# Optimization experiments

Hardware: AMD Instinct MI355X
Metric: run time of the kernel (lower is better)

## Reference

```python
import jax, jax.numpy as jnp
import numpy as np

# QuadraticConv2DTranspose reconstruction:
#   1) bed-of-nails upsample by stride s (pixels at i*s, zeros elsewhere), padded by k-1
#      so a VALID conv yields output H*s x W*s ('same' transpose-conv geometry)
#   2) per-(pixel, in_channel) flattened k*k patch p (K=k*k values)
#   3) quadratic features: upper-triangular outer products p_i*p_j (K*(K+1)/2 terms),
#      plus linear terms p (K) and a bias term 1  -> L = 55 for k=3
#   4) contract features against flat_kernel [1,1,L,Cin,Cout]

KH = 3            # kernel height/width
STRIDE = 2
KK = KH * KH      # flattened patch size per channel = 9
L = KK * (KK + 1) // 2 + KK + 1  # 45 quad + 9 linear + 1 bias = 55
B, H, W, CIN, COUT = 8, 32, 32, 64, 64


def setup_inputs() -> dict:
    key = jax.random.key(0)
    k1, k2 = jax.random.split(key)
    x = jax.random.normal(k1, (B, H, W, CIN), dtype=jnp.float32)
    flat_kernel = jax.random.normal(k2, (1, 1, L, CIN, COUT), dtype=jnp.float32) * 0.02
    return {"x": x, "flat_kernel": flat_kernel}


def _quadratic_conv_transpose(x, flat_kernel):
    b, h, w, c = x.shape
    k, s = KH, STRIDE
    pad = k - 1
    pb = pad // 2
    # bed-of-nails upsampling into a pre-padded buffer: [B, H*s + k-1, W*s + k-1, C]
    up = jnp.zeros((b, h * s + pad, w * s + pad, c), dtype=x.dtype)
    up = up.at[:, pb:pb + h * s:s, pb:pb + w * s:s, :].set(x)
    # im2col: [B, Ho, Wo, C*K] with feature dim ordered (C, kh, kw)
    patches = jax.lax.conv_general_dilated_patches(
        up, (k, k), (1, 1), 'VALID',
        dimension_numbers=('NHWC', 'HWIO', 'NHWC'))
    ho, wo = h * s, w * s
    p = patches.reshape(b, ho, wo, c, KK)  # per-channel flattened patch
    iu, ju = np.triu_indices(KK)           # 45 upper-triangular index pairs
    quad = p[..., iu] * p[..., ju]         # [B,Ho,Wo,C,45]
    ones = jnp.ones(p.shape[:-1] + (1,), dtype=p.dtype)
    feat = jnp.concatenate([quad, p, ones], axis=-1)  # [B,Ho,Wo,C,L]
    # contract over (L, Cin) against kernel [L,Cin,Cout]
    return jnp.einsum('bhwcl,lco->bhwo', feat, flat_kernel[0, 0])


def reference(x, flat_kernel):
    return _quadratic_conv_transpose(x, flat_kernel)
```

## Files before the change

kernel.cpp:

```cpp
#include <hip/hip_runtime.h>
#include <stdint.h>


namespace {
constexpr int kBiasL = 54;
}

typedef __attribute__((ext_vector_type(8))) short short8;
typedef __attribute__((ext_vector_type(4))) float floatx4;

__device__ __forceinline__ short f2bf(float f) {
  union { float f; uint32_t u; } v{f};
  uint32_t u = v.u;
  u += 0x7fffu + ((u >> 16) & 1u);
  return (short)(u >> 16);
}

template <int CLS> struct CI;
template <> struct CI<0> {
  static constexpr int NV = 1, NF = 2;
  static constexpr int L[NF] = {30, 49};
  static constexpr int A[NF] = {0, 0};
  static constexpr int Bb[NF] = {0, 1};
  static constexpr int DY[NV] = {0};
  static constexpr int DX[NV] = {0};
};
template <> struct CI<1> {
  static constexpr int NV = 2, NF = 5;
  static constexpr int L[NF] = {24, 26, 35, 48, 50};
  static constexpr int A[NF] = {0, 0, 1, 0, 1};
  static constexpr int Bb[NF] = {0, 1, 1, 2, 2};
  static constexpr int DY[NV] = {0, 0};
  static constexpr int DX[NV] = {0, 1};
};
template <> struct CI<2> {
  static constexpr int NV = 2, NF = 5;
  static constexpr int L[NF] = {9, 15, 42, 46, 52};
  static constexpr int A[NF] = {0, 0, 1, 0, 1};
  static constexpr int Bb[NF] = {0, 1, 1, 2, 2};
  static constexpr int DY[NV] = {0, 1};
  static constexpr int DX[NV] = {0, 0};
};
template <> struct CI<3> {
  static constexpr int NV = 4, NF = 14;
  static constexpr int L[NF] = {0, 2, 6, 8, 17, 21, 23, 39, 41, 44, 45, 47, 51, 53};
  static constexpr int A[NF] = {0, 0, 0, 0, 1, 1, 1, 2, 2, 3, 0, 1, 2, 3};
  static constexpr int Bb[NF] = {0, 1, 2, 3, 1, 2, 3, 2, 3, 3, 4, 4, 4, 4};
  static constexpr int DY[NV] = {0, 0, 1, 1};
  static constexpr int DX[NV] = {0, 1, 0, 1};
};

__global__ __launch_bounds__(256) void bias_kernel(const float* __restrict__ kern,
                                                   float* __restrict__ bias) {
  __shared__ float sb[4][64];
  const int o = threadIdx.x & 63;
  const int part = threadIdx.x >> 6;
  float s = 0.f;
#pragma unroll
  for (int c = 0; c < 16; ++c)
    s += kern[(kBiasL * 64 + part * 16 + c) * 64 + o];
  sb[part][o] = s;
  __syncthreads();
  if (part == 0) bias[o] = sb[0][o] + sb[1][o] + sb[2][o] + sb[3][o];
}

template <int CLS>
__device__ __forceinline__ void body(const float* __restrict__ x,
                                     const float* __restrict__ kern,
                                     const float* __restrict__ bias,
                                     float* __restrict__ out, int b, int hi0,
                                     int wi0, float (&sX)[45][36],
                                     short (&sBt)[2][64][40]) {
  using I = CI<CLS>;
  constexpr int NV = I::NV, NF = I::NF;
  const int tid = threadIdx.x;
  const int wave = tid >> 6, lane = tid & 63;
  const int quad = lane >> 4, l16 = lane & 15;
  const int mb = (wave & 1) * 16;
  const int nh = (wave >> 1) * 32;
  const int m = mb + l16;
  const int ph = m >> 3, pw = m & 7;
  const int c8 = quad * 8;

  floatx4 acc[2];
#pragma unroll
  for (int nt = 0; nt < 2; ++nt) {
    const float bv = bias[nh + nt * 16 + l16];
    acc[nt] = floatx4{bv, bv, bv, bv};
  }

  int fidx = 0;
  for (int chalf = 0; chalf < 2; ++chalf) {
    const int c0 = chalf * 32;
    for (int i = tid; i < 45 * 8; i += 256) {
      const int pos = i >> 3, c4 = (i & 7) * 4;
      const int hr = hi0 + pos / 9, wc = wi0 + pos % 9;
      float4 v = make_float4(0.f, 0.f, 0.f, 0.f);
      if (hr < 32 && wc < 32)
        v = *(const float4*)&x[(((b * 32) + hr) * 32 + wc) * 64 + c0 + c4];
      *(float4*)&sX[pos][c4] = v;
    }
    __syncthreads();
    float vpl[NV][8];
#pragma unroll
    for (int j = 0; j < NV; ++j) {
      const int pa = (ph + I::DY[j]) * 9 + (pw + I::DX[j]);
      *(float4*)&vpl[j][0] = *(const float4*)&sX[pa][c8];
      *(float4*)&vpl[j][4] = *(const float4*)&sX[pa][c8 + 4];
    }
    for (int f = 0; f < NF; ++f, ++fidx) {
      short(&sB)[64][40] = sBt[fidx & 1];
      {
        const int n = tid & 63, kkg = (tid >> 6) * 8;
        const float* src = &kern[((I::L[f] * 64) + c0 + kkg) * 64 + n];
        short8 wv;
#pragma unroll
        for (int j = 0; j < 8; ++j) wv[j] = f2bf(src[j * 64]);
        *(short8*)&sB[n][kkg] = wv;
      }
      __syncthreads();
      short8 afrag;
#pragma unroll
      for (int j = 0; j < 8; ++j) {
        const float v = (I::Bb[f] == NV) ? vpl[I::A[f]][j]
                                         : vpl[I::A[f]][j] * vpl[I::Bb[f]][j];
        afrag[j] = f2bf(v);
      }
#pragma unroll
      for (int nt = 0; nt < 2; ++nt) {
        const short8 bfrag = *(const short8*)&sB[nh + nt * 16 + l16][c8];
        acc[nt] =
            __builtin_amdgcn_mfma_f32_16x16x32_bf16(afrag, bfrag, acc[nt], 0, 0, 0);
      }
    }
  }

  constexpr int rh = CLS >> 1, rw = CLS & 1;
#pragma unroll
  for (int nt = 0; nt < 2; ++nt) {
    const int n = nh + nt * 16 + l16;
#pragma unroll
    for (int r = 0; r < 4; ++r) {
      const int mm = mb + quad * 4 + r;
      const int hi = hi0 + (mm >> 3), wi = wi0 + (mm & 7);
      const int ho = 2 * hi + rh, wo = 2 * wi + rw;
      out[(((b * 64) + ho) * 64 + wo) * 64 + n] = acc[nt][r];
    }
  }
}

__global__ __launch_bounds__(256) void qct_main(const float* __restrict__ x,
                                                const float* __restrict__ kern,
                                                const float* __restrict__ bias,
                                                float* __restrict__ out) {
  __shared__ float sX[45][36];
  __shared__ short sBt[2][64][40];
  const int bid = blockIdx.x;
  int cls, blk;
  if (bid < 256)      { cls = 3; blk = bid; }
  else if (bid < 512) { cls = 1; blk = bid - 256; }
  else if (bid < 768) { cls = 2; blk = bid - 512; }
  else                { cls = 0; blk = bid - 768; }
  const int b = blk >> 5, tile = blk & 31;
  const int hi0 = (tile >> 2) * 4;
  const int wi0 = (tile & 3) * 8;
  switch (cls) {
    case 0: body<0>(x, kern, bias, out, b, hi0, wi0, sX, sBt); break;
    case 1: body<1>(x, kern, bias, out, b, hi0, wi0, sX, sBt); break;
    case 2: body<2>(x, kern, bias, out, b, hi0, wi0, sX, sBt); break;
    case 3: body<3>(x, kern, bias, out, b, hi0, wi0, sX, sBt); break;
  }
}

extern "C" void kernel_launch(void* const* d_in, const int* in_sizes, int n_in,
                              void* d_out, int out_size, void* d_ws,
                              size_t ws_size, hipStream_t stream) {
  const float* x = (const float*)d_in[0];
  const float* kern = (const float*)d_in[1];
  float* out = (float*)d_out;
  float* bias = (float*)d_ws;

  bias_kernel<<<1, 256, 0, stream>>>(kern, bias);
  qct_main<<<1024, 256, 0, stream>>>(x, kern, bias, out);
}
```

Baseline: 73.67 us.

## Pre-convert weights to transposed bf16 and load MFMA B-fragments straight from global

Adds a prep kernel that converts the whole flat kernel to bf16, transposed to [L][Cout][Cin], and also computes the bias sum. The main kernel now reads B fragments directly from global/L2 instead of converting fp32 weights into a double-buffered LDS tile with a barrier per feature. It also loads all 64 input channels into LDS once, removing the per-half reload and most syncthreads. This cuts repeated fp32->bf16 conversion and synchronisation, at the cost of a larger prep kernel, uncoalesced-ish global B loads and a launch-bounds occupancy hint.

```diff
diff --git a/kernel.cpp b/kernel.cpp
--- a/kernel.cpp
+++ b/kernel.cpp
@@ -2,11 +2,8 @@
 #include <stdint.h>
 
 
-namespace {
-constexpr int kBiasL = 54;
-}
-
 typedef __attribute__((ext_vector_type(8))) short short8;
+typedef __attribute__((ext_vector_type(4))) short short4v;
 typedef __attribute__((ext_vector_type(4))) float floatx4;
 
 __device__ __forceinline__ short f2bf(float f) {
@@ -50,27 +47,37 @@
   static constexpr int DX[NV] = {0, 1, 0, 1};
 };
 
-__global__ __launch_bounds__(256) void bias_kernel(const float* __restrict__ kern,
-                                                   float* __restrict__ bias) {
-  __shared__ float sb[4][64];
-  const int o = threadIdx.x & 63;
-  const int part = threadIdx.x >> 6;
-  float s = 0.f;
-#pragma unroll
-  for (int c = 0; c < 16; ++c)
-    s += kern[(kBiasL * 64 + part * 16 + c) * 64 + o];
-  sb[part][o] = s;
+__global__ __launch_bounds__(256) void prep_w(const float* __restrict__ kern,
+                                              short* __restrict__ wt,
+                                              float* __restrict__ bias) {
+  __shared__ float s[64][65];
+  const int l = blockIdx.x;
+  const int tid = threadIdx.x;
+  for (int i = tid; i < 4096; i += 256)
+    s[i >> 6][i & 63] = kern[(l << 12) + i];
   __syncthreads();
-  if (part == 0) bias[o] = sb[0][o] + sb[1][o] + sb[2][o] + sb[3][o];
+  if (l == 54 && tid < 64) {
+    float a = 0.f;
+    for (int c = 0; c < 64; ++c) a += s[c][tid];
+    bias[tid] = a;
+  }
+  for (int i = tid; i < 1024; i += 256) {
+    const int n = i >> 4, c4 = (i & 15) * 4;
+    short4v v;
+    v[0] = f2bf(s[c4 + 0][n]);
+    v[1] = f2bf(s[c4 + 1][n]);
+    v[2] = f2bf(s[c4 + 2][n]);
+    v[3] = f2bf(s[c4 + 3][n]);
+    *(short4v*)&wt[((l << 6) + n) * 64 + c4] = v;
+  }
 }
 
 template <int CLS>
 __device__ __forceinline__ void body(const float* __restrict__ x,
-                                     const float* __restrict__ kern,
+                                     const short* __restrict__ wt,
                                      const float* __restrict__ bias,
                                      float* __restrict__ out, int b, int hi0,
-                                     int wi0, float (&sX)[45][36],
-                                     short (&sBt)[2][64][40]) {
+                                     int wi0, float (&sX)[45][68]) {
   using I = CI<CLS>;
   constexpr int NV = I::NV, NF = I::NF;
   const int tid = threadIdx.x;
@@ -82,6 +89,15 @@
   const int ph = m >> 3, pw = m & 7;
   const int c8 = quad * 8;
 
+  for (int i = tid; i < 720; i += 256) {
+    const int pos = i >> 4, c4 = (i & 15) * 4;
+    const int hr = hi0 + pos / 9, wc = wi0 + pos % 9;
+    float4 v = make_float4(0.f, 0.f, 0.f, 0.f);
+    if (hr < 32 && wc < 32)
+      v = *(const float4*)&x[(((b * 32) + hr) * 32 + wc) * 64 + c4];
+    *(float4*)&sX[pos][c4] = v;
+  }
+
   floatx4 acc[2];
 #pragma unroll
   for (int nt = 0; nt < 2; ++nt) {
@@ -89,49 +105,34 @@
     acc[nt] = floatx4{bv, bv, bv, bv};
   }
 
-  int fidx = 0;
+  __syncthreads();
+
+  float vpl[NV][16];
+#pragma unroll
+  for (int j = 0; j < NV; ++j) {
+    const int pa = (ph + I::DY[j]) * 9 + (pw + I::DX[j]);
+    *(float4*)&vpl[j][0] = *(const float4*)&sX[pa][c8];
+    *(float4*)&vpl[j][4] = *(const float4*)&sX[pa][c8 + 4];
+    *(float4*)&vpl[j][8] = *(const float4*)&sX[pa][32 + c8];
+    *(float4*)&vpl[j][12] = *(const float4*)&sX[pa][32 + c8 + 4];
+  }
+
+#pragma unroll
   for (int chalf = 0; chalf < 2; ++chalf) {
-    const int c0 = chalf * 32;
-    for (int i = tid; i < 45 * 8; i += 256) {
-      const int pos = i >> 3, c4 = (i & 7) * 4;
-      const int hr = hi0 + pos / 9, wc = wi0 + pos % 9;
-      float4 v = make_float4(0.f, 0.f, 0.f, 0.f);
-      if (hr < 32 && wc < 32)
-        v = *(const float4*)&x[(((b * 32) + hr) * 32 + wc) * 64 + c0 + c4];
-      *(float4*)&sX[pos][c4] = v;
-    }
-    __syncthreads();
-    float vpl[NV][8];
 #pragma unroll
-    for (int j = 0; j < NV; ++j) {
-      const int pa = (ph + I::DY[j]) * 9 + (pw + I::DX[j]);
-      *(float4*)&vpl[j][0] = *(const float4*)&sX[pa][c8];
-      *(float4*)&vpl[j][4] = *(const float4*)&sX[pa][c8 + 4];
-    }
-    for (int f = 0; f < NF; ++f, ++fidx) {
-      short(&sB)[64][40] = sBt[fidx & 1];
-      {
-        const int n = tid & 63, kkg = (tid >> 6) * 8;
-        const float* src = &kern[((I::L[f] * 64) + c0 + kkg) * 64 + n];
-        short8 wv;
-#pragma unroll
-        for (int j = 0; j < 8; ++j) wv[j] = f2bf(src[j * 64]);
-        *(short8*)&sB[n][kkg] = wv;
-      }
-      __syncthreads();
-      short8 afrag;
+    for (int f = 0; f < NF; ++f) {
+      const short* wr = wt + (I::L[f] * 64) * 64 + chalf * 32 + c8;
+      const short8 b0 = *(const short8*)&wr[(nh + l16) * 64];
+      const short8 b1 = *(const short8*)&wr[(nh + 16 + l16) * 64];
+      short8 af;
 #pragma unroll
       for (int j = 0; j < 8; ++j) {
-        const float v = (I::Bb[f] == NV) ? vpl[I::A[f]][j]
-                                         : vpl[I::A[f]][j] * vpl[I::Bb[f]][j];
-        afrag[j] = f2bf(v);
+        const float va = vpl[I::A[f]][chalf * 8 + j];
+        const float v = (I::Bb[f] == NV) ? va : va * vpl[I::Bb[f]][chalf * 8 + j];
+        af[j] = f2bf(v);
       }
-#pragma unroll
-      for (int nt = 0; nt < 2; ++nt) {
-        const short8 bfrag = *(const short8*)&sB[nh + nt * 16 + l16][c8];
-        acc[nt] =
-            __builtin_amdgcn_mfma_f32_16x16x32_bf16(afrag, bfrag, acc[nt], 0, 0, 0);
-      }
+      acc[0] = __builtin_amdgcn_mfma_f32_16x16x32_bf16(af, b0, acc[0], 0, 0, 0);
+      acc[1] = __builtin_amdgcn_mfma_f32_16x16x32_bf16(af, b1, acc[1], 0, 0, 0);
     }
   }
 
@@ -149,12 +150,11 @@
   }
 }
 
-__global__ __launch_bounds__(256) void qct_main(const float* __restrict__ x,
-                                                const float* __restrict__ kern,
-                                                const float* __restrict__ bias,
-                                                float* __restrict__ out) {
-  __shared__ float sX[45][36];
-  __shared__ short sBt[2][64][40];
+__global__ __launch_bounds__(256, 4) void qct_main(const float* __restrict__ x,
+                                                   const short* __restrict__ wt,
+                                                   const float* __restrict__ bias,
+                                                   float* __restrict__ out) {
+  __shared__ float sX[45][68];
   const int bid = blockIdx.x;
   int cls, blk;
   if (bid < 256)      { cls = 3; blk = bid; }
@@ -165,10 +165,10 @@
   const int hi0 = (tile >> 2) * 4;
   const int wi0 = (tile & 3) * 8;
   switch (cls) {
-    case 0: body<0>(x, kern, bias, out, b, hi0, wi0, sX, sBt); break;
-    case 1: body<1>(x, kern, bias, out, b, hi0, wi0, sX, sBt); break;
-    case 2: body<2>(x, kern, bias, out, b, hi0, wi0, sX, sBt); break;
-    case 3: body<3>(x, kern, bias, out, b, hi0, wi0, sX, sBt); break;
+    case 0: body<0>(x, wt, bias, out, b, hi0, wi0, sX); break;
+    case 1: body<1>(x, wt, bias, out, b, hi0, wi0, sX); break;
+    case 2: body<2>(x, wt, bias, out, b, hi0, wi0, sX); break;
+    case 3: body<3>(x, wt, bias, out, b, hi0, wi0, sX); break;
   }
 }
 
@@ -178,8 +178,9 @@
   const float* x = (const float*)d_in[0];
   const float* kern = (const float*)d_in[1];
   float* out = (float*)d_out;
-  float* bias = (float*)d_ws;
+  short* wt = (short*)d_ws;
+  float* bias = (float*)((char*)d_ws + 55 * 64 * 64 * 2);
 
-  bias_kernel<<<1, 256, 0, stream>>>(kern, bias);
-  qct_main<<<1024, 256, 0, stream>>>(x, kern, bias, out);
+  prep_w<<<55, 256, 0, stream>>>(kern, wt, bias);
+  qct_main<<<1024, 256, 0, stream>>>(x, wt, bias, out);
 }
```

New measurement: 75.00 us. No clear change (+1.8%).
